# Kernel tuning notes

Hardware: AMD Instinct MI355X
Metric: run time of the kernel (lower is better)

## Reference

```python
import jax, jax.numpy as jnp
import numpy as np
from jax import lax

K = 20        # cfgs.k: knn size for edge-conv graph features
OUT_K = 8     # cfgs.out_k: knn size for output aggregation
OUT_DIM = 256
EPS = 1e-5    # BatchNorm eps (torch default), training-mode batch stats


def _bn(y, g, b, axes):
    m = y.mean(axes, keepdims=True)
    v = y.var(axes, keepdims=True)  # biased var, as torch BN uses for normalization
    return (y - m) * lax.rsqrt(v + EPS) * g + b


def _graph_feature(x, k):
    # x: [B,N,C] -> [B,N,k,2C] = concat(neighbor - center, center)
    xx = jnp.sum(x * x, axis=-1)                          # [B,N]
    inner = jnp.einsum('bnc,bmc->bnm', x, x)              # [B,N,N]
    neg_d = 2.0 * inner - xx[:, :, None] - xx[:, None, :]  # -||xi-xj||^2
    idx = lax.top_k(neg_d, k)[1]                          # [B,N,k] nearest (incl. self)
    nbr = jax.vmap(lambda p, i: p[i])(x, idx)             # [B,N,k,C]
    ctr = jnp.broadcast_to(x[:, :, None, :], nbr.shape)
    return jnp.concatenate([nbr - ctr, ctr], axis=-1)


def _edgeconv(x, w, g, b):
    # x: [B,N,C] -> [B,N,O]; conv2d 1x1 (no bias) + BN + LeakyReLU(0.2) + max over k
    f = _graph_feature(x, K)                              # [B,N,K,2C]
    y = jnp.einsum('bnkc,oc->bnko', f, w)
    y = jax.nn.leaky_relu(_bn(y, g, b, (0, 1, 2)), 0.2)
    return y.max(axis=2)


def _fps(pts, npoint):
    # furthest point sampling, start at index 0 (pointnet2 convention). pts: [B,N,3]
    B, N, _ = pts.shape
    d0 = jnp.full((B, N), 1e10, pts.dtype)
    first = jnp.zeros((B,), jnp.int32)

    def step(carry, _):
        dist, last = carry
        lp = jnp.take_along_axis(pts, last[:, None, None], axis=1)  # [B,1,3]
        d = jnp.sum((pts - lp) ** 2, axis=-1)
        dist = jnp.minimum(dist, d)
        nxt = jnp.argmax(dist, axis=-1).astype(jnp.int32)
        return (dist, nxt), nxt

    _, rest = lax.scan(step, (d0, first), None, length=npoint - 1)
    return jnp.concatenate([first[:, None], rest.T], axis=1)  # [B,npoint]


def reference(x, w1, g1, b1, w2, g2, b2, wf, gf, bf, wc, gc, bc):
    B, N, _ = x.shape
    # edge-conv block 1: 6 -> 64
    x1 = _edgeconv(x, w1, g1, b1)                         # [B,N,64]
    n1 = N // 2
    _ = _fps(x, n1)  # points[1]; unused when f_layer == c_layer == 2
    # edge-conv block 2: 128 -> 64
    x2 = _edgeconv(x1, w2, g2, b2)                        # [B,N,64]
    n2 = n1 // 2
    idx2 = _fps(x, n2)                                    # [B,M]
    p2 = jax.vmap(lambda p, i: p[i])(x, idx2)             # [B,M,3]
    # KNN(support=x points, query=p2): indices of OUT_K nearest support points
    d = jnp.sum((p2[:, :, None, :] - x[:, None, :, :]) ** 2, axis=-1)  # [B,M,N]
    knn_idx = lax.top_k(-d, OUT_K)[1]                     # [B,M,OUT_K]
    # gather neighbor features from x2 and mean over neighbors
    agg = jax.vmap(lambda f, i: f[i])(x2, knn_idx).mean(axis=2)        # [B,M,64]
    f_out = _bn(jnp.einsum('bmc,oc->bmo', agg, wf), gf, bf, (0, 1)).transpose(0, 2, 1)
    c_out = _bn(jnp.einsum('bmc,oc->bmo', agg, wc), gc, bc, (0, 1)).transpose(0, 2, 1)
    mask = jnp.ones((B, n2), dtype=bool)
    return (f_out, c_out, p2, p2, mask, mask)


def setup_inputs() -> dict:
    key = jax.random.key(0)
    ks = jax.random.split(key, 6)
    B, N = 4, 4096
    x = jax.random.normal(ks[0], (B, N, 3), jnp.float32)
    def w(k, o, c):
        return jax.random.normal(k, (o, c), jnp.float32) / np.sqrt(c)
    return {
        'x': x,
        'w1': w(ks[1], 64, 6),   'g1': jnp.ones(64),  'b1': jnp.zeros(64),
        'w2': w(ks[2], 64, 128), 'g2': jnp.ones(64),  'b2': jnp.zeros(64),
        'wf': w(ks[3], OUT_DIM, 64), 'gf': jnp.ones(OUT_DIM), 'bf': jnp.zeros(OUT_DIM),
        'wc': w(ks[4], OUT_DIM, 64), 'gc': jnp.ones(OUT_DIM), 'bc': jnp.zeros(OUT_DIM),
    }
```

## Files before the change

kernel.cpp:

```cpp
#include <hip/hip_runtime.h>

#define WB 4
#define WN 4096
#define WKNN 20
#define WM 1024
#define WOUTK 8
#define WOD 256
#define BEPS 1e-5f

typedef unsigned long long u64;
typedef unsigned int u32;

#define ACC_F    0
#define IDX1_I   2048
#define IDX2NN_I 329728
#define IDX2_I   657408
#define X1_F     661504
#define XX1_F    1710080
#define X2_F     1726464

#define O_F   0
#define O_C   1048576
#define O_P2A 2097152
#define O_P2B 2109440
#define O_M0  2121728
#define O_M1  2125824

__device__ __forceinline__ u64 shflx64(u64 v, int m){
    int lo = __shfl_xor((int)(u32)(v & 0xFFFFFFFFull), m, 64);
    int hi = __shfl_xor((int)(u32)(v >> 32), m, 64);
    return ((u64)(u32)hi << 32) | (u32)lo;
}
__device__ __forceinline__ u32 encf(float d){
    u32 u = __float_as_uint(d);
    return (u & 0x80000000u) ? ~u : (u | 0x80000000u);
}
template<int L>
__device__ __forceinline__ void ins(u64* lst, u64 key){
    if (key < lst[L-1]){
        #pragma unroll
        for (int j = 0; j < L; ++j){
            u64 a = lst[j];
            u64 mn = key < a ? key : a;
            u64 mx = key < a ? a : key;
            lst[j] = mn; key = mx;
        }
    }
}

template<int CTRL, int RM>
__device__ __forceinline__ void dppsel(double& k, float& x, float& y, float& z){
    int lo = __double2loint(k), hi = __double2hiint(k);
    int slo = __builtin_amdgcn_update_dpp(lo, lo, CTRL, RM, 0xF, false);
    int shi = __builtin_amdgcn_update_dpp(hi, hi, CTRL, RM, 0xF, false);
    int sx = __builtin_amdgcn_update_dpp(__float_as_int(x), __float_as_int(x), CTRL, RM, 0xF, false);
    int sy = __builtin_amdgcn_update_dpp(__float_as_int(y), __float_as_int(y), CTRL, RM, 0xF, false);
    int sz = __builtin_amdgcn_update_dpp(__float_as_int(z), __float_as_int(z), CTRL, RM, 0xF, false);
    double ok = __hiloint2double(shi, slo);
    bool t = ok > k;
    k = t ? ok : k;
    x = t ? __int_as_float(sx) : x;
    y = t ? __int_as_float(sy) : y;
    z = t ? __int_as_float(sz) : z;
}

__global__ __launch_bounds__(512,1)
void k1_fps_knn1(const float* __restrict__ x, float* __restrict__ out,
                 int* __restrict__ idx1, int* __restrict__ idx2){
    __shared__ float px[WN], py[WN], pz[WN];
    __shared__ double wk[2][4];
    __shared__ float wx4[2][4], wy4[2][4], wz4[2][4];
    int tid = threadIdx.x;
    if (blockIdx.x < 4){
        int b = (int)blockIdx.x;
        const float* xb = x + b*WN*3;
        if (tid >= 256){
            for (int i = tid-256; i < WM; i += 256){
                out[O_M0 + b*WM + i] = 1.0f;
                out[O_M1 + b*WM + i] = 1.0f;
            }
            for (int it=1; it<WM; ++it) __syncthreads();
        } else {
            float ptx[16],pty[16],ptz[16],dst[16];
            #pragma unroll
            for (int j=0;j<16;++j){
                int p = tid + j*256;
                ptx[j]=xb[p*3]; pty[j]=xb[p*3+1]; ptz[j]=xb[p*3+2];
                dst[j]=1e10f;
            }
            float lx=xb[0], ly=xb[1], lz=xb[2];
            if (tid==0){
                idx2[b*WM] = 0;
                int o3 = (b*WM)*3;
                out[O_P2A+o3]=lx; out[O_P2A+o3+1]=ly; out[O_P2A+o3+2]=lz;
                out[O_P2B+o3]=lx; out[O_P2B+o3+1]=ly; out[O_P2B+o3+2]=lz;
            }
            int w = tid>>6, lane = tid&63;
            for (int it=1; it<WM; ++it){
                double bk = -1.0; float bx=lx, by=ly, bz=lz;
                #pragma unroll
                for (int j=0;j<16;++j){
                    float dx=ptx[j]-lx, dy=pty[j]-ly, dz=ptz[j]-lz;
                    float d = dx*dx + dy*dy + dz*dz;
                    d = fminf(dst[j], d); dst[j] = d;
                    double kd = __hiloint2double(__float_as_int(d),
                                                 4095 - (tid + j*256));
                    bool t = kd > bk;
                    bk = t?kd:bk; bx = t?ptx[j]:bx; by = t?pty[j]:by; bz = t?ptz[j]:bz;
                }
                dppsel<0x111,0xF>(bk,bx,by,bz);
                dppsel<0x112,0xF>(bk,bx,by,bz);
                dppsel<0x114,0xF>(bk,bx,by,bz);
                dppsel<0x118,0xF>(bk,bx,by,bz);
                dppsel<0x142,0xA>(bk,bx,by,bz);
                dppsel<0x143,0xC>(bk,bx,by,bz);
                int ib = it & 1;
                if (lane==63){ wk[ib][w]=bk; wx4[ib][w]=bx; wy4[ib][w]=by; wz4[ib][w]=bz; }
                __syncthreads();
                int e = lane & 3;
                double gk = wk[ib][e];
                float gx = wx4[ib][e], gy = wy4[ib][e], gz = wz4[ib][e];
                dppsel<0xB1,0xF>(gk,gx,gy,gz);
                dppsel<0x4E,0xF>(gk,gx,gy,gz);
                lx = gx; ly = gy; lz = gz;
                if (tid==0){
                    int last = 4095 - (int)(u32)__double2loint(gk);
                    idx2[b*WM+it] = last;
                    int o3 = (b*WM+it)*3;
                    out[O_P2A+o3]=lx; out[O_P2A+o3+1]=ly; out[O_P2A+o3+2]=lz;
                    out[O_P2B+o3]=lx; out[O_P2B+o3+1]=ly; out[O_P2B+o3+2]=lz;
                }
            }
        }
    } else {
        int kb = (int)blockIdx.x - 4;
        int b = kb >> 9;
        const float* xb = x + b*WN*3;
        for (int i = tid; i < WN*3; i += 512){
            float v = xb[i];
            int n = i/3, c = i - n*3;
            if (c==0) px[n]=v; else if (c==1) py[n]=v; else pz[n]=v;
        }
        __syncthreads();
        int wid = tid>>6, lane = tid&63;
        int n = (kb & 511)*8 + wid;
        int grow = b*WN + n;
        float qx=px[n], qy=py[n], qz=pz[n];
        float qq = qx*qx+qy*qy+qz*qz;
        u64 lst[WKNN];
        #pragma unroll
        for (int j=0;j<WKNN;++j) lst[j]=~0ull;
        for (int t=0;t<64;++t){
            int c = lane + t*64;
            float sx=px[c], sy=py[c], sz=pz[c];
            float ss = sx*sx+sy*sy+sz*sz;
            float inner = qx*sx+qy*sy+qz*sz;
            float nd = (2.0f*inner - qq) - ss;
            u64 key = ((u64)(0xFFFFFFFFu - encf(nd))<<32) | (u32)c;
            ins<WKNN>(lst, key);
        }
        int ob = grow*WKNN;
        for (int r=0;r<WKNN;++r){
            u64 k = lst[0];
            #pragma unroll
            for (int m=32;m;m>>=1){ u64 o = shflx64(k,m); k = o<k?o:k; }
            if (lane==0) idx1[ob+r] = (int)(k & 0xFFFFFFFFu);
            if (lst[0]==k){
                #pragma unroll
                for (int j=0;j<WKNN-1;++j) lst[j]=lst[j+1];
                lst[WKNN-1]=~0ull;
            }
        }
    }
}

__global__ __launch_bounds__(256,1)
void k2_ec1_stats(const float* __restrict__ x, const float* __restrict__ w1,
                  const int* __restrict__ idx1, float* __restrict__ acc){
    __shared__ float as[64], aq[64];
    int tid = threadIdx.x;
    if (tid < 64){ as[tid]=0.f; aq[tid]=0.f; }
    __syncthreads();
    int cg = tid & 7, sg = tid >> 3;
    int chb = cg*8;
    float w[8][6];
    #pragma unroll
    for (int i=0;i<8;++i){
        #pragma unroll
        for (int j=0;j<6;++j) w[i][j] = w1[(chb+i)*6+j];
    }
    float s[8]={0,0,0,0,0,0,0,0}, q[8]={0,0,0,0,0,0,0,0};
    int s0 = (int)blockIdx.x*1024 + sg*32;
    for (int i=0;i<32;++i){
        int smp = s0+i;
        int bn = smp/WKNN;
        int j = idx1[smp];
        int bb = bn >> 12;
        const float* ct = x + bn*3;
        const float* nb = x + (bb*WN + j)*3;
        float c0=ct[0],c1=ct[1],c2=ct[2];
        float f0=nb[0]-c0, f1=nb[1]-c1, f2=nb[2]-c2;
        #pragma unroll
        for (int c=0;c<8;++c){
            float y = w[c][0]*f0 + w[c][1]*f1 + w[c][2]*f2
                    + w[c][3]*c0 + w[c][4]*c1 + w[c][5]*c2;
            s[c] += y; q[c] = fmaf(y,y,q[c]);
        }
    }
    #pragma unroll
    for (int c=0;c<8;++c){ atomicAdd(&as[chb+c], s[c]); atomicAdd(&aq[chb+c], q[c]); }
    __syncthreads();
    if (tid < 64){ atomicAdd(&acc[tid], as[tid]); atomicAdd(&acc[64+tid], aq[tid]); }
}

__global__ __launch_bounds__(256,1)
void k4_ec1_apply(const float* __restrict__ x, const float* __restrict__ w1,
                  const float* __restrict__ g1, const float* __restrict__ b1,
                  const int* __restrict__ idx1, const float* __restrict__ acc,
                  float* __restrict__ x1){
    int lin = (int)blockIdx.x*256 + threadIdx.x;
    int row = lin >> 3, cg = lin & 7, chb = cg*8;
    int bb = row >> 12;
    const float Pinv = 1.0f/(float)(WB*WN*WKNN);
    float aa[8], cc[8], w[8][6];
    #pragma unroll
    for (int i=0;i<8;++i){
        int ch = chb+i;
        float mean = acc[ch]*Pinv;
        float var  = acc[64+ch]*Pinv - mean*mean;
        float rstd = rsqrtf(var + BEPS);
        aa[i] = g1[ch]*rstd;
        cc[i] = b1[ch] - mean*aa[i];
        #pragma unroll
        for (int j=0;j<6;++j) w[i][j]=w1[ch*6+j];
    }
    const float* ct = x + row*3;
    float c0=ct[0],c1=ct[1],c2=ct[2];
    float mx[8];
    #pragma unroll
    for (int i=0;i<8;++i) mx[i] = -1e30f;
    for (int k=0;k<WKNN;++k){
        int j = idx1[row*WKNN+k];
        const float* nb = x + (bb*WN + j)*3;
        float f0=nb[0]-c0, f1=nb[1]-c1, f2=nb[2]-c2;
        #pragma unroll
        for (int c=0;c<8;++c){
            float y = w[c][0]*f0 + w[c][1]*f1 + w[c][2]*f2
                    + w[c][3]*c0 + w[c][4]*c1 + w[c][5]*c2;
            float v = fmaf(y, aa[c], cc[c]);
            v = fmaxf(v, 0.2f*v);
            mx[c] = fmaxf(mx[c], v);
        }
    }
    #pragma unroll
    for (int c=0;c<8;++c) x1[row*64 + chb + c] = mx[c];
}

__global__ __launch_bounds__(256,1)
void k5_xx1(const float* __restrict__ x1, float* __restrict__ xx1){
    int wid = threadIdx.x>>6, lane = threadIdx.x&63;
    int row = (int)blockIdx.x*4 + wid;
    float v = x1[row*64+lane];
    float s = v*v;
    #pragma unroll
    for (int m=32;m;m>>=1) s += __shfl_xor(s,m,64);
    if (lane==0) xx1[row]=s;
}

__global__ __launch_bounds__(512,1)
void k6_knn2(const float* __restrict__ x1, const float* __restrict__ xx1,
             int* __restrict__ idx2nn){
    __shared__ __align__(16) float Qt[64*64];
    __shared__ __align__(16) float St[128*68];
    __shared__ float Sxx[128];
    float* Dt = St;
    int tid = threadIdx.x, wid = tid>>6, lane = tid&63;
    int b = (int)blockIdx.x >> 6, qt = (int)blockIdx.x & 63;
    const float* xb = x1 + b*WN*64;
    for (int i=tid; i<64*16; i+=512){
        int r = i>>4, c4 = i&15;
        *(float4*)&Qt[r*64 + c4*4] = *(const float4*)&xb[(qt*64+r)*64 + c4*4];
    }
    float qxx[8];
    #pragma unroll
    for (int i=0;i<8;++i) qxx[i] = xx1[b*WN + qt*64 + wid*8 + i];
    u64 lst[WKNN];
    #pragma unroll
    for (int j=0;j<WKNN;++j) lst[j]=~0ull;
    int sq = tid>>3, seg = tid&7;
    for (int ct=0; ct<32; ++ct){
        int cb = ct*128;
        __syncthreads();
        for (int i=tid; i<128*16; i+=512){
            int r=i>>4, c4=i&15;
            *(float4*)&St[r*68 + c4*4] = *(const float4*)&xb[(cb+r)*64 + c4*4];
        }
        if (tid < 128) Sxx[tid] = xx1[b*WN + cb + tid];
        __syncthreads();
        float acc[8][2];
        #pragma unroll
        for (int i=0;i<8;++i){ acc[i][0]=0.f; acc[i][1]=0.f; }
        #pragma unroll 4
        for (int d4=0; d4<16; ++d4){
            float4 s0 = *(const float4*)&St[lane*68 + d4*4];
            float4 s1 = *(const float4*)&St[(lane+64)*68 + d4*4];
            #pragma unroll
            for (int i=0;i<8;++i){
                float4 qv = *(const float4*)&Qt[(wid*8+i)*64 + d4*4];
                acc[i][0] += qv.x*s0.x + qv.y*s0.y + qv.z*s0.z + qv.w*s0.w;
                acc[i][1] += qv.x*s1.x + qv.y*s1.y + qv.z*s1.z + qv.w*s1.w;
            }
        }
        __syncthreads();
        float sx0 = Sxx[lane], sx1 = Sxx[lane+64];
        #pragma unroll
        for (int i=0;i<8;++i){
            int r = wid*8+i;
            Dt[r*132 + lane]      = (2.0f*acc[i][0] - qxx[i]) - sx0;
            Dt[r*132 + lane + 64] = (2.0f*acc[i][1] - qxx[i]) - sx1;
        }
        __syncthreads();
        #pragma unroll
        for (int m=0;m<16;++m){
            int col = seg*16+m;
            float nd = Dt[sq*132 + col];
            u64 key = ((u64)(0xFFFFFFFFu - encf(nd))<<32) | (u32)(cb+col);
            ins<WKNN>(lst,key);
        }
    }
    int ob = (b*WN + qt*64 + sq)*WKNN;
    for (int r=0;r<WKNN;++r){
        u64 k = lst[0];
        #pragma unroll
        for (int m=4;m;m>>=1){ u64 o=shflx64(k,m); k = o<k?o:k; }
        if ((tid&7)==0) idx2nn[ob+r] = (int)(k & 0xFFFFFFFFu);
        if (lst[0]==k){
            #pragma unroll
            for (int j=0;j<WKNN-1;++j) lst[j]=lst[j+1];
            lst[WKNN-1]=~0ull;
        }
    }
}

__global__ __launch_bounds__(512,1)
void k7_ec2_stats(const float* __restrict__ x1, const float* __restrict__ w2,
                  const int* __restrict__ idx2nn, float* __restrict__ acc){
    __shared__ __align__(16) float wsm[64*128];
    __shared__ float as[64], aq[64];
    int tid = threadIdx.x, wid = tid>>6, lane = tid&63;
    for (int i=tid; i<2048; i+=512)
        *(float4*)&wsm[i*4] = *(const float4*)&w2[i*4];
    if (tid<64){ as[tid]=0.f; aq[tid]=0.f; }
    __syncthreads();
    int row = (int)blockIdx.x*64 + lane;
    int b = row >> 12;
    const float* xr  = x1 + row*64;
    const float* xbb = x1 + b*WN*64;
    float ss[8]={0,0,0,0,0,0,0,0}, qs[8]={0,0,0,0,0,0,0,0};
    for (int kc=0; kc<5; ++kc){
        int jj[4];
        #pragma unroll
        for (int kk=0;kk<4;++kk) jj[kk] = idx2nn[row*WKNN + kc*4 + kk];
        float av[8][4];
        #pragma unroll
        for (int c=0;c<8;++c){ av[c][0]=0;av[c][1]=0;av[c][2]=0;av[c][3]=0; }
        #pragma unroll 4
        for (int dc=0; dc<16; ++dc){
            float4 cv = *(const float4*)&xr[dc*4];
            float4 fv[4];
            #pragma unroll
            for (int kk=0;kk<4;++kk){
                float4 nv = *(const float4*)&xbb[jj[kk]*64 + dc*4];
                fv[kk].x=nv.x-cv.x; fv[kk].y=nv.y-cv.y; fv[kk].z=nv.z-cv.z; fv[kk].w=nv.w-cv.w;
            }
            #pragma unroll
            for (int c=0;c<8;++c){
                float4 wv = *(const float4*)&wsm[(wid*8+c)*128 + dc*4];
                #pragma unroll
                for (int kk=0;kk<4;++kk)
                    av[c][kk] += wv.x*fv[kk].x + wv.y*fv[kk].y + wv.z*fv[kk].z + wv.w*fv[kk].w;
            }
        }
        #pragma unroll 4
        for (int dc=16; dc<32; ++dc){
            float4 cv = *(const float4*)&xr[(dc-16)*4];
            #pragma unroll
            for (int c=0;c<8;++c){
                float4 wv = *(const float4*)&wsm[(wid*8+c)*128 + dc*4];
                float dv = wv.x*cv.x + wv.y*cv.y + wv.z*cv.z + wv.w*cv.w;
                #pragma unroll
                for (int kk=0;kk<4;++kk) av[c][kk] += dv;
            }
        }
        #pragma unroll
        for (int c=0;c<8;++c){
            #pragma unroll
            for (int kk=0;kk<4;++kk){ ss[c]+=av[c][kk]; qs[c]=fmaf(av[c][kk],av[c][kk],qs[c]); }
        }
    }
    #pragma unroll
    for (int c=0;c<8;++c){ atomicAdd(&as[wid*8+c], ss[c]); atomicAdd(&aq[wid*8+c], qs[c]); }
    __syncthreads();
    if (tid<64){ atomicAdd(&acc[128+tid], as[tid]); atomicAdd(&acc[192+tid], aq[tid]); }
}

__global__ __launch_bounds__(512,1)
void k9_ec2_apply(const float* __restrict__ x1, const float* __restrict__ w2,
                  const float* __restrict__ g2, const float* __restrict__ b2,
                  const int* __restrict__ idx2nn, const float* __restrict__ acc,
                  float* __restrict__ x2){
    __shared__ __align__(16) float wsm[64*128];
    int tid = threadIdx.x, wid = tid>>6, lane = tid&63;
    for (int i=tid; i<2048; i+=512)
        *(float4*)&wsm[i*4] = *(const float4*)&w2[i*4];
    __syncthreads();
    const float Pinv = 1.0f/(float)(WB*WN*WKNN);
    float aa[8], cc[8];
    #pragma unroll
    for (int c=0;c<8;++c){
        int ch = wid*8+c;
        float mean = acc[128+ch]*Pinv;
        float var  = acc[192+ch]*Pinv - mean*mean;
        float rstd = rsqrtf(var + BEPS);
        aa[c] = g2[ch]*rstd;
        cc[c] = b2[ch] - mean*aa[c];
    }
    int row = (int)blockIdx.x*64 + lane;
    int b = row>>12;
    const float* xr  = x1 + row*64;
    const float* xbb = x1 + b*WN*64;
    float mx[8];
    #pragma unroll
    for (int c=0;c<8;++c) mx[c] = -1e30f;
    for (int kc=0;kc<5;++kc){
        int jj[4];
        #pragma unroll
        for (int kk=0;kk<4;++kk) jj[kk]=idx2nn[row*WKNN+kc*4+kk];
        float av[8][4];
        #pragma unroll
        for (int c=0;c<8;++c){ av[c][0]=0;av[c][1]=0;av[c][2]=0;av[c][3]=0; }
        #pragma unroll 4
        for (int dc=0;dc<16;++dc){
            float4 cv = *(const float4*)&xr[dc*4];
            float4 fv[4];
            #pragma unroll
            for (int kk=0;kk<4;++kk){
                float4 nv = *(const float4*)&xbb[jj[kk]*64 + dc*4];
                fv[kk].x=nv.x-cv.x; fv[kk].y=nv.y-cv.y; fv[kk].z=nv.z-cv.z; fv[kk].w=nv.w-cv.w;
            }
            #pragma unroll
            for (int c=0;c<8;++c){
                float4 wv = *(const float4*)&wsm[(wid*8+c)*128 + dc*4];
                #pragma unroll
                for (int kk=0;kk<4;++kk)
                    av[c][kk] += wv.x*fv[kk].x + wv.y*fv[kk].y + wv.z*fv[kk].z + wv.w*fv[kk].w;
            }
        }
        #pragma unroll 4
        for (int dc=16;dc<32;++dc){
            float4 cv = *(const float4*)&xr[(dc-16)*4];
            #pragma unroll
            for (int c=0;c<8;++c){
                float4 wv = *(const float4*)&wsm[(wid*8+c)*128 + dc*4];
                float dv = wv.x*cv.x + wv.y*cv.y + wv.z*cv.z + wv.w*cv.w;
                #pragma unroll
                for (int kk=0;kk<4;++kk) av[c][kk] += dv;
            }
        }
        #pragma unroll
        for (int c=0;c<8;++c){
            #pragma unroll
            for (int kk=0;kk<4;++kk){
                float v = fmaf(av[c][kk], aa[c], cc[c]);
                v = fmaxf(v, 0.2f*v);
                mx[c] = fmaxf(mx[c], v);
            }
        }
    }
    #pragma unroll
    for (int c=0;c<8;++c) x2[row*64 + wid*8 + c] = mx[c];
}

__global__ __launch_bounds__(256,1)
void k10_out(const float* __restrict__ x, const float* __restrict__ x2,
             const int* __restrict__ idx2, const float* __restrict__ wf,
             const float* __restrict__ wc, float* __restrict__ out,
             float* __restrict__ acc){
    __shared__ float px[WN], py[WN], pz[WN];
    __shared__ __align__(16) float aggs[4][64];
    __shared__ float sacc[1024];
    int tid=threadIdx.x, wid=tid>>6, lane=tid&63;
    int b = (int)blockIdx.x >> 6;
    int mb = ((int)blockIdx.x & 63)*16;
    const float* xb = x + b*WN*3;
    for (int i=tid;i<WN*3;i+=256){
        float v=xb[i]; int n=i/3,c=i-n*3;
        if(c==0)px[n]=v; else if(c==1)py[n]=v; else pz[n]=v;
    }
    for (int i=tid;i<1024;i+=256) sacc[i]=0.f;
    __syncthreads();
    for (int qq=0;qq<4;++qq){
        int m = mb + wid*4 + qq;
        int pi = idx2[b*WM+m];
        float qx=px[pi], qy=py[pi], qz=pz[pi];
        u64 lst[WOUTK];
        #pragma unroll
        for (int j=0;j<WOUTK;++j) lst[j]=~0ull;
        for (int t=0;t<64;++t){
            int c = lane + t*64;
            float dx=qx-px[c], dy=qy-py[c], dz=qz-pz[c];
            float d = dx*dx+dy*dy+dz*dz;
            u64 key = ((u64)encf(d)<<32) | (u32)c;
            ins<WOUTK>(lst,key);
        }
        int jr[WOUTK];
        #pragma unroll
        for (int r=0;r<WOUTK;++r){
            u64 k=lst[0];
            #pragma unroll
            for (int mm=32;mm;mm>>=1){ u64 o=shflx64(k,mm); k = o<k?o:k; }
            jr[r] = (int)(k&0xFFFFFFFFu);
            if (lst[0]==k){
                #pragma unroll
                for (int j=0;j<WOUTK-1;++j) lst[j]=lst[j+1];
                lst[WOUTK-1]=~0ull;
            }
        }
        float a = 0.f;
        #pragma unroll
        for (int r=0;r<WOUTK;++r) a += x2[(b*WN + jr[r])*64 + lane];
        a *= 0.125f;
        aggs[wid][lane] = a;
        __syncthreads();
        #pragma unroll
        for (int i=0;i<4;++i){
            int o = lane + 64*i;
            const float4* wfp = (const float4*)(wf + o*64);
            const float4* wcp = (const float4*)(wc + o*64);
            float af=0.f, ac=0.f;
            #pragma unroll
            for (int d4=0;d4<16;++d4){
                float4 avv = *(const float4*)&aggs[wid][d4*4];
                float4 w1v = wfp[d4];
                float4 w2v = wcp[d4];
                af += w1v.x*avv.x + w1v.y*avv.y + w1v.z*avv.z + w1v.w*avv.w;
                ac += w2v.x*avv.x + w2v.y*avv.y + w2v.z*avv.z + w2v.w*avv.w;
            }
            out[O_F + (b*WOD + o)*WM + m] = af;
            out[O_C + (b*WOD + o)*WM + m] = ac;
            atomicAdd(&sacc[o],       af);
            atomicAdd(&sacc[256+o],   af*af);
            atomicAdd(&sacc[512+o],   ac);
            atomicAdd(&sacc[768+o],   ac*ac);
        }
        __syncthreads();
    }
    for (int i=tid;i<1024;i+=256) atomicAdd(&acc[256+i], sacc[i]);
}

__global__ __launch_bounds__(256,1)
void k12_final(const float* __restrict__ acc,
               const float* __restrict__ gf, const float* __restrict__ bf,
               const float* __restrict__ gc, const float* __restrict__ bc,
               float* __restrict__ out){
    int t = (int)blockIdx.x*256 + threadIdx.x;
    int half = t >> 20;
    int r = t & 0xFFFFF;
    int o = (r >> 10) & 255;
    const float Pinv = 1.0f/4096.0f;
    float sum = acc[(half?768:256) + o];
    float sq  = acc[(half?1024:512) + o];
    float mean = sum*Pinv;
    float var  = sq*Pinv - mean*mean;
    float rstd = rsqrtf(var + BEPS);
    float g  = half ? gc[o] : gf[o];
    float bb = half ? bc[o] : bf[o];
    float y = out[t];
    out[t] = (y-mean)*rstd*g + bb;
}

extern "C" void kernel_launch(void* const* d_in, const int* in_sizes, int n_in,
                              void* d_out, int out_size, void* d_ws, size_t ws_size,
                              hipStream_t stream){
    const float* x  = (const float*)d_in[0];
    const float* w1 = (const float*)d_in[1];
    const float* g1 = (const float*)d_in[2];
    const float* b1 = (const float*)d_in[3];
    const float* w2 = (const float*)d_in[4];
    const float* g2 = (const float*)d_in[5];
    const float* b2 = (const float*)d_in[6];
    const float* wf = (const float*)d_in[7];
    const float* gf = (const float*)d_in[8];
    const float* bf = (const float*)d_in[9];
    const float* wc = (const float*)d_in[10];
    const float* gc = (const float*)d_in[11];
    const float* bc = (const float*)d_in[12];
    float* out = (float*)d_out;
    float* wsf = (float*)d_ws;
    int*   wsi = (int*)d_ws;
    float* ACC    = wsf + ACC_F;
    int*   idx1   = wsi + IDX1_I;
    int*   idx2nn = wsi + IDX2NN_I;
    int*   idx2   = wsi + IDX2_I;
    float* x1     = wsf + X1_F;
    float* xx1    = wsf + XX1_F;
    float* x2     = wsf + X2_F;

    hipMemsetAsync(ACC, 0, 1280*sizeof(float), stream);
    k1_fps_knn1 <<<2052,512,0,stream>>>(x,out,idx1,idx2);
    k2_ec1_stats<<<320, 256, 0,stream>>>(x,w1,idx1,ACC);
    k4_ec1_apply<<<512, 256, 0,stream>>>(x,w1,g1,b1,idx1,ACC,x1);
    k5_xx1      <<<4096,256, 0,stream>>>(x1,xx1);
    k6_knn2     <<<256, 512, 0,stream>>>(x1,xx1,idx2nn);
    k7_ec2_stats<<<256, 512, 0,stream>>>(x1,w2,idx2nn,ACC);
    k9_ec2_apply<<<256, 512, 0,stream>>>(x1,w2,g2,b2,idx2nn,ACC,x2);
    k10_out     <<<256, 256, 0,stream>>>(x,x2,idx2,wf,wc,out,ACC);
    k12_final   <<<8192,256, 0,stream>>>(ACC,gf,bf,gc,bc,out);
}
```

Baseline: 2.004 ms.

## Widen FPS to 1024 threads, buffer results in LDS, fuse xx1 into ec1 apply

The furthest-point-sampling blocks now use all 1024 threads, each handling 4 points instead of 16. The reduction gains a tree-select step and a two-level DPP cross-wave merge over 16 waves, shortening the serial per-iteration chain. Sampled indices and coordinates are kept in shared memory and written out coalesced at the end, rather than by thread 0 every iteration. The separate xx1 norm kernel is folded into k4_ec1_apply via a shuffle reduction, dropping one launch and one pass over x1, and the knn1 blocks are reshaped to 16 waves each.

```diff
diff --git a/kernel.cpp b/kernel.cpp
--- a/kernel.cpp
+++ b/kernel.cpp
@@ -48,6 +48,11 @@
     }
 }
 
+__device__ __forceinline__ void sel2(double& ka, float& xa, float& ya, float& za,
+                                     double kb, float xb, float yb, float zb){
+    bool t = kb > ka;
+    ka = t?kb:ka; xa = t?xb:xa; ya = t?yb:ya; za = t?zb:za;
+}
 template<int CTRL, int RM>
 __device__ __forceinline__ void dppsel(double& k, float& x, float& y, float& z){
     int lo = __double2loint(k), hi = __double2hiint(k);
@@ -64,95 +69,100 @@
     z = t ? __int_as_float(sz) : z;
 }
 
-__global__ __launch_bounds__(512,1)
+struct SmemA { float px[WN], py[WN], pz[WN]; };
+struct SmemF { double wk[2][16]; float wx[2][16], wy[2][16], wz[2][16];
+               float bx[WM], by[WM], bz[WM]; int bidx[WM]; };
+union SmemK1 { SmemA a; SmemF f; };
+
+__global__ __launch_bounds__(1024,1)
 void k1_fps_knn1(const float* __restrict__ x, float* __restrict__ out,
                  int* __restrict__ idx1, int* __restrict__ idx2){
-    __shared__ float px[WN], py[WN], pz[WN];
-    __shared__ double wk[2][4];
-    __shared__ float wx4[2][4], wy4[2][4], wz4[2][4];
+    __shared__ SmemK1 sm;
     int tid = threadIdx.x;
     if (blockIdx.x < 4){
         int b = (int)blockIdx.x;
         const float* xb = x + b*WN*3;
-        if (tid >= 256){
-            for (int i = tid-256; i < WM; i += 256){
-                out[O_M0 + b*WM + i] = 1.0f;
-                out[O_M1 + b*WM + i] = 1.0f;
-            }
-            for (int it=1; it<WM; ++it) __syncthreads();
-        } else {
-            float ptx[16],pty[16],ptz[16],dst[16];
-            #pragma unroll
-            for (int j=0;j<16;++j){
-                int p = tid + j*256;
-                ptx[j]=xb[p*3]; pty[j]=xb[p*3+1]; ptz[j]=xb[p*3+2];
-                dst[j]=1e10f;
-            }
-            float lx=xb[0], ly=xb[1], lz=xb[2];
+        float ptx[4],pty[4],ptz[4],dst[4];
+        #pragma unroll
+        for (int j=0;j<4;++j){
+            int p = tid + j*1024;
+            ptx[j]=xb[p*3]; pty[j]=xb[p*3+1]; ptz[j]=xb[p*3+2];
+            dst[j]=1e10f;
+        }
+        float lx=xb[0], ly=xb[1], lz=xb[2];
+        if (tid==0){ sm.f.bidx[0]=0; sm.f.bx[0]=lx; sm.f.by[0]=ly; sm.f.bz[0]=lz; }
+        int w = tid>>6, lane = tid&63;
+        int base = 4095 - tid;
+        for (int it=1; it<WM; ++it){
+            double kk[4];
+            #pragma unroll
+            for (int j=0;j<4;++j){
+                float dx=ptx[j]-lx, dy=pty[j]-ly, dz=ptz[j]-lz;
+                float d = dx*dx + dy*dy + dz*dz;
+                d = fminf(dst[j], d); dst[j] = d;
+                kk[j] = __hiloint2double(__float_as_int(d), base - j*1024);
+            }
+            double m0=kk[0], m1=kk[2];
+            float ax0=ptx[0],ay0=pty[0],az0=ptz[0];
+            float ax1=ptx[2],ay1=pty[2],az1=ptz[2];
+            sel2(m0,ax0,ay0,az0, kk[1],ptx[1],pty[1],ptz[1]);
+            sel2(m1,ax1,ay1,az1, kk[3],ptx[3],pty[3],ptz[3]);
+            sel2(m0,ax0,ay0,az0, m1,ax1,ay1,az1);
+            double bk=m0; float bx=ax0, by=ay0, bz=az0;
+            dppsel<0x111,0xF>(bk,bx,by,bz);
+            dppsel<0x112,0xF>(bk,bx,by,bz);
+            dppsel<0x114,0xF>(bk,bx,by,bz);
+            dppsel<0x118,0xF>(bk,bx,by,bz);
+            dppsel<0x142,0xA>(bk,bx,by,bz);
+            dppsel<0x143,0xC>(bk,bx,by,bz);
+            int ib = it & 1;
+            if (lane==63){ sm.f.wk[ib][w]=bk; sm.f.wx[ib][w]=bx; sm.f.wy[ib][w]=by; sm.f.wz[ib][w]=bz; }
+            __syncthreads();
+            int e = lane & 15;
+            double gk = sm.f.wk[ib][e];
+            float gx = sm.f.wx[ib][e], gy = sm.f.wy[ib][e], gz = sm.f.wz[ib][e];
+            dppsel<0x128,0xF>(gk,gx,gy,gz);
+            dppsel<0x124,0xF>(gk,gx,gy,gz);
+            dppsel<0x4E,0xF>(gk,gx,gy,gz);
+            dppsel<0xB1,0xF>(gk,gx,gy,gz);
+            lx = gx; ly = gy; lz = gz;
             if (tid==0){
-                idx2[b*WM] = 0;
-                int o3 = (b*WM)*3;
-                out[O_P2A+o3]=lx; out[O_P2A+o3+1]=ly; out[O_P2A+o3+2]=lz;
-                out[O_P2B+o3]=lx; out[O_P2B+o3+1]=ly; out[O_P2B+o3+2]=lz;
-            }
-            int w = tid>>6, lane = tid&63;
-            for (int it=1; it<WM; ++it){
-                double bk = -1.0; float bx=lx, by=ly, bz=lz;
-                #pragma unroll
-                for (int j=0;j<16;++j){
-                    float dx=ptx[j]-lx, dy=pty[j]-ly, dz=ptz[j]-lz;
-                    float d = dx*dx + dy*dy + dz*dz;
-                    d = fminf(dst[j], d); dst[j] = d;
-                    double kd = __hiloint2double(__float_as_int(d),
-                                                 4095 - (tid + j*256));
-                    bool t = kd > bk;
-                    bk = t?kd:bk; bx = t?ptx[j]:bx; by = t?pty[j]:by; bz = t?ptz[j]:bz;
-                }
-                dppsel<0x111,0xF>(bk,bx,by,bz);
-                dppsel<0x112,0xF>(bk,bx,by,bz);
-                dppsel<0x114,0xF>(bk,bx,by,bz);
-                dppsel<0x118,0xF>(bk,bx,by,bz);
-                dppsel<0x142,0xA>(bk,bx,by,bz);
-                dppsel<0x143,0xC>(bk,bx,by,bz);
-                int ib = it & 1;
-                if (lane==63){ wk[ib][w]=bk; wx4[ib][w]=bx; wy4[ib][w]=by; wz4[ib][w]=bz; }
-                __syncthreads();
-                int e = lane & 3;
-                double gk = wk[ib][e];
-                float gx = wx4[ib][e], gy = wy4[ib][e], gz = wz4[ib][e];
-                dppsel<0xB1,0xF>(gk,gx,gy,gz);
-                dppsel<0x4E,0xF>(gk,gx,gy,gz);
-                lx = gx; ly = gy; lz = gz;
-                if (tid==0){
-                    int last = 4095 - (int)(u32)__double2loint(gk);
-                    idx2[b*WM+it] = last;
-                    int o3 = (b*WM+it)*3;
-                    out[O_P2A+o3]=lx; out[O_P2A+o3+1]=ly; out[O_P2A+o3+2]=lz;
-                    out[O_P2B+o3]=lx; out[O_P2B+o3+1]=ly; out[O_P2B+o3+2]=lz;
-                }
-            }
+                sm.f.bidx[it] = 4095 - (int)(u32)__double2loint(gk);
+                sm.f.bx[it]=lx; sm.f.by[it]=ly; sm.f.bz[it]=lz;
+            }
+        }
+        __syncthreads();
+        for (int i=tid;i<WM;i+=1024){
+            idx2[b*WM+i] = sm.f.bidx[i];
+            out[O_M0 + b*WM + i] = 1.0f;
+            out[O_M1 + b*WM + i] = 1.0f;
+        }
+        for (int i=tid;i<WM*3;i+=1024){
+            int p=i/3, c=i-p*3;
+            float v = (c==0)?sm.f.bx[p]:((c==1)?sm.f.by[p]:sm.f.bz[p]);
+            out[O_P2A + b*WM*3 + i] = v;
+            out[O_P2B + b*WM*3 + i] = v;
         }
     } else {
-        int kb = (int)blockIdx.x - 4;
-        int b = kb >> 9;
+        int wid = tid>>6, lane = tid&63;
+        int b = (int)((blockIdx.x - 4) >> 8);
         const float* xb = x + b*WN*3;
-        for (int i = tid; i < WN*3; i += 512){
+        for (int i = tid; i < WN*3; i += 1024){
             float v = xb[i];
             int n = i/3, c = i - n*3;
-            if (c==0) px[n]=v; else if (c==1) py[n]=v; else pz[n]=v;
-        }
-        __syncthreads();
-        int wid = tid>>6, lane = tid&63;
-        int n = (kb & 511)*8 + wid;
-        int grow = b*WN + n;
-        float qx=px[n], qy=py[n], qz=pz[n];
+            if (c==0) sm.a.px[n]=v; else if (c==1) sm.a.py[n]=v; else sm.a.pz[n]=v;
+        }
+        __syncthreads();
+        int grow = ((int)blockIdx.x-4)*16 + wid;
+        int n = grow & 4095;
+        float qx=sm.a.px[n], qy=sm.a.py[n], qz=sm.a.pz[n];
         float qq = qx*qx+qy*qy+qz*qz;
         u64 lst[WKNN];
         #pragma unroll
         for (int j=0;j<WKNN;++j) lst[j]=~0ull;
         for (int t=0;t<64;++t){
             int c = lane + t*64;
-            float sx=px[c], sy=py[c], sz=pz[c];
+            float sx=sm.a.px[c], sy=sm.a.py[c], sz=sm.a.pz[c];
             float ss = sx*sx+sy*sy+sz*sz;
             float inner = qx*sx+qy*sy+qz*sz;
             float nd = (2.0f*inner - qq) - ss;
@@ -217,7 +227,7 @@
 void k4_ec1_apply(const float* __restrict__ x, const float* __restrict__ w1,
                   const float* __restrict__ g1, const float* __restrict__ b1,
                   const int* __restrict__ idx1, const float* __restrict__ acc,
-                  float* __restrict__ x1){
+                  float* __restrict__ x1, float* __restrict__ xx1){
     int lin = (int)blockIdx.x*256 + threadIdx.x;
     int row = lin >> 3, cg = lin & 7, chb = cg*8;
     int bb = row >> 12;
@@ -252,19 +262,13 @@
             mx[c] = fmaxf(mx[c], v);
         }
     }
-    #pragma unroll
-    for (int c=0;c<8;++c) x1[row*64 + chb + c] = mx[c];
-}
-
-__global__ __launch_bounds__(256,1)
-void k5_xx1(const float* __restrict__ x1, float* __restrict__ xx1){
-    int wid = threadIdx.x>>6, lane = threadIdx.x&63;
-    int row = (int)blockIdx.x*4 + wid;
-    float v = x1[row*64+lane];
-    float s = v*v;
-    #pragma unroll
-    for (int m=32;m;m>>=1) s += __shfl_xor(s,m,64);
-    if (lane==0) xx1[row]=s;
+    float sq2 = 0.f;
+    #pragma unroll
+    for (int c=0;c<8;++c){ x1[row*64 + chb + c] = mx[c]; sq2 = fmaf(mx[c],mx[c],sq2); }
+    sq2 += __shfl_xor(sq2,1,64);
+    sq2 += __shfl_xor(sq2,2,64);
+    sq2 += __shfl_xor(sq2,4,64);
+    if (cg==0) xx1[row] = sq2;
 }
 
 __global__ __launch_bounds__(512,1)
@@ -297,9 +301,9 @@
         }
         if (tid < 128) Sxx[tid] = xx1[b*WN + cb + tid];
         __syncthreads();
-        float acc[8][2];
-        #pragma unroll
-        for (int i=0;i<8;++i){ acc[i][0]=0.f; acc[i][1]=0.f; }
+        float a2[8][2];
+        #pragma unroll
+        for (int i=0;i<8;++i){ a2[i][0]=0.f; a2[i][1]=0.f; }
         #pragma unroll 4
         for (int d4=0; d4<16; ++d4){
             float4 s0 = *(const float4*)&St[lane*68 + d4*4];
@@ -307,8 +311,8 @@
             #pragma unroll
             for (int i=0;i<8;++i){
                 float4 qv = *(const float4*)&Qt[(wid*8+i)*64 + d4*4];
-                acc[i][0] += qv.x*s0.x + qv.y*s0.y + qv.z*s0.z + qv.w*s0.w;
-                acc[i][1] += qv.x*s1.x + qv.y*s1.y + qv.z*s1.z + qv.w*s1.w;
+                a2[i][0] += qv.x*s0.x + qv.y*s0.y + qv.z*s0.z + qv.w*s0.w;
+                a2[i][1] += qv.x*s1.x + qv.y*s1.y + qv.z*s1.z + qv.w*s1.w;
             }
         }
         __syncthreads();
@@ -316,8 +320,8 @@
         #pragma unroll
         for (int i=0;i<8;++i){
             int r = wid*8+i;
-            Dt[r*132 + lane]      = (2.0f*acc[i][0] - qxx[i]) - sx0;
-            Dt[r*132 + lane + 64] = (2.0f*acc[i][1] - qxx[i]) - sx1;
+            Dt[r*132 + lane]      = (2.0f*a2[i][0] - qxx[i]) - sx0;
+            Dt[r*132 + lane + 64] = (2.0f*a2[i][1] - qxx[i]) - sx1;
         }
         __syncthreads();
         #pragma unroll
@@ -607,10 +611,9 @@
     float* x2     = wsf + X2_F;
 
     hipMemsetAsync(ACC, 0, 1280*sizeof(float), stream);
-    k1_fps_knn1 <<<2052,512,0,stream>>>(x,out,idx1,idx2);
+    k1_fps_knn1 <<<1028,1024,0,stream>>>(x,out,idx1,idx2);
     k2_ec1_stats<<<320, 256, 0,stream>>>(x,w1,idx1,ACC);
-    k4_ec1_apply<<<512, 256, 0,stream>>>(x,w1,g1,b1,idx1,ACC,x1);
-    k5_xx1      <<<4096,256, 0,stream>>>(x1,xx1);
+    k4_ec1_apply<<<512, 256, 0,stream>>>(x,w1,g1,b1,idx1,ACC,x1,xx1);
     k6_knn2     <<<256, 512, 0,stream>>>(x1,xx1,idx2nn);
     k7_ec2_stats<<<256, 512, 0,stream>>>(x1,w2,idx2nn,ACC);
     k9_ec2_apply<<<256, 512, 0,stream>>>(x1,w2,g2,b2,idx2nn,ACC,x2);
```

Result: slower. 2.675 ms (+33.5%).
